# Performance work log

Hardware: AMD Instinct MI355X
Metric: run time of the kernel (lower is better)

## Reference

```python
import jax, jax.numpy as jnp
import numpy as np

N, T, E, H, V = 32768, 20, 50, 50, 200
PAD = 0

def setup_inputs() -> dict:
    key = jax.random.key(0)
    ks = jax.random.split(key, 11)
    s = 1.0 / np.sqrt(H)  # torch LSTM init scale
    return {
        "char_indices": jax.random.randint(ks[0], (N, T), 0, V, dtype=jnp.int32),
        "word_lengths": jax.random.randint(ks[1], (N,), 0, T + 1, dtype=jnp.int32),
        "emb": jax.random.normal(ks[2], (V, E), jnp.float32) * 0.1,
        "W_ih_f": jax.random.normal(ks[3], (4 * H, E), jnp.float32) * s,
        "W_hh_f": jax.random.normal(ks[4], (4 * H, H), jnp.float32) * s,
        "b_ih_f": jax.random.normal(ks[5], (4 * H,), jnp.float32) * s,
        "b_hh_f": jax.random.normal(ks[6], (4 * H,), jnp.float32) * s,
        "W_ih_b": jax.random.normal(ks[7], (4 * H, E), jnp.float32) * s,
        "W_hh_b": jax.random.normal(ks[8], (4 * H, H), jnp.float32) * s,
        "b_ih_b": jax.random.normal(ks[9], (4 * H,), jnp.float32) * s,
        "b_hh_b": jax.random.normal(ks[10], (4 * H,), jnp.float32) * s,
    }

def _run_dir(x, lengths, W_ih, W_hh, b_ih, b_hh, reverse):
    # x: [N,T,E]; returns final hidden state [N,H] at the word's true boundary.
    n = x.shape[0]
    xg = jnp.einsum('nte,ge->ntg', x, W_ih) + b_ih + b_hh  # [N,T,4H]
    def step(carry, t):
        h, c = carry
        g = xg[:, t] + h @ W_hh.T  # [N,4H]
        i, f, gg, o = jnp.split(g, 4, axis=-1)
        c_new = jax.nn.sigmoid(f) * c + jax.nn.sigmoid(i) * jnp.tanh(gg)
        h_new = jax.nn.sigmoid(o) * jnp.tanh(c_new)
        valid = (t < lengths)[:, None]  # only update inside the word
        return (jnp.where(valid, h_new, h), jnp.where(valid, c_new, c)), None
    ts = jnp.arange(T - 1, -1, -1) if reverse else jnp.arange(T)
    z = jnp.zeros((n, W_hh.shape[1]), x.dtype)
    (h, _), _ = jax.lax.scan(step, (z, z), ts)
    return h

def reference(char_indices, word_lengths, emb, W_ih_f, W_hh_f, b_ih_f, b_hh_f,
              W_ih_b, W_hh_b, b_ih_b, b_hh_b):
    emb = emb.at[PAD].set(0.0)  # padding_idx row is zero
    x = emb[char_indices]  # [N,T,E]
    h_f = _run_dir(x, word_lengths, W_ih_f, W_hh_f, b_ih_f, b_hh_f, reverse=False)
    h_b = _run_dir(x, word_lengths, W_ih_b, W_hh_b, b_ih_b, b_hh_b, reverse=True)
    return jnp.concatenate([h_f, h_b], axis=-1)  # [N, 2H]
```

## Files before the change

### kernel.cpp

```cpp
#include <hip/hip_runtime.h>


#define TT    20
#define HH    50
#define VV    200
#define TILES 13
#define GSTR  212
#define GSH   (VV * GSTR)
#define WSH   (TILES * 16 * 64)
#define NW    32768
#define NB_G  332
#define NB_W  104
#define NB_H  128

typedef __attribute__((ext_vector_type(8))) short bf16x8;
typedef __attribute__((ext_vector_type(4))) short s16x4;
typedef __attribute__((ext_vector_type(4))) float f32x4;

__device__ __forceinline__ float frcp(float x) { return __builtin_amdgcn_rcpf(x); }
__device__ __forceinline__ float fsig(float x) { return frcp(1.0f + __expf(-x)); }
__device__ __forceinline__ float ftanhf(float x) { return 1.0f - 2.0f * frcp(1.0f + __expf(2.0f * x)); }

__device__ __forceinline__ short f2bf(float x) {
    unsigned b = __builtin_bit_cast(unsigned, x);
    unsigned r = (b + 0x7FFFu + ((b >> 16) & 1u)) >> 16;
    return (short)r;
}
__device__ __forceinline__ float bf2f(short s) {
    return __builtin_bit_cast(float, ((unsigned)(unsigned short)s) << 16);
}

__global__ void k_prep(const float* __restrict__ emb,
                       const float* __restrict__ Wih_f, const float* __restrict__ bih_f,
                       const float* __restrict__ bhh_f,
                       const float* __restrict__ Wih_b, const float* __restrict__ bih_b,
                       const float* __restrict__ bhh_b,
                       const float* __restrict__ Whh_f, const float* __restrict__ Whh_b,
                       const int* __restrict__ lens,
                       short* __restrict__ Gimg, short* __restrict__ Wimg,
                       int* __restrict__ cnt) {
    int blk = blockIdx.x;
    int tid = threadIdx.x;
    if (blk < NB_G) {
        int idx = blk * 256 + tid;
        if (idx >= 2 * GSH) return;
        int d = idx / GSH;
        int rem = idx % GSH;
        int v = rem / GSTR;
        int u = (rem % GSTR) >> 2;
        int g = idx & 3;
        if (u >= HH) { Gimg[idx] = 0; return; }
        int r = g * HH + u;
        const float* Wih = d ? Wih_b : Wih_f;
        const float* bih = d ? bih_b : bih_f;
        const float* bhh = d ? bhh_b : bhh_f;
        float s = bih[r] + bhh[r];
        if (v != 0) {
            #pragma unroll 10
            for (int e = 0; e < HH; ++e) s = fmaf(emb[v * HH + e], Wih[r * HH + e], s);
        }
        Gimg[idx] = f2bf(s);
    } else if (blk < NB_G + NB_W) {
        int idx = (blk - NB_G) * 256 + tid;
        if (idx >= 2 * WSH) return;
        int d = idx / WSH;
        int e = idx % WSH;
        int t = e >> 10, m = (e >> 6) & 15, k = e & 63;
        int u = 4 * t + (m >> 2), g = m & 3;
        const float* Whh = d ? Whh_b : Whh_f;
        float val = (k < HH && u < HH) ? Whh[(g * HH + u) * HH + k] : 0.0f;
        int ksw = (k & 7) | (((k >> 3) ^ (m & 7)) << 3);
        Wimg[d * WSH + (e & ~63) + ksw] = f2bf(val);
    } else {
        int hb = blk - NB_G - NB_W;
        __shared__ int hcnt[21];
        if (tid < 21) hcnt[tid] = 0;
        __syncthreads();
        atomicAdd(&hcnt[lens[hb * 256 + tid]], 1);
        __syncthreads();
        if (tid < 21) cnt[hb * 21 + tid] = hcnt[tid];
    }
}

__global__ void k_scan(const int* __restrict__ cnt, int* __restrict__ offs) {
    __shared__ int tot[21], start[21];
    int t = threadIdx.x;
    if (t < 21) {
        int s = 0;
        for (int b = 0; b < NB_H; ++b) s += cnt[b * 21 + t];
        tot[t] = s;
    }
    __syncthreads();
    if (t == 0) {
        int acc = 0;
        for (int L = 20; L >= 0; --L) { start[L] = acc; acc += tot[L]; }
    }
    __syncthreads();
    if (t < 21) {
        int acc = start[t];
        for (int b = 0; b < NB_H; ++b) { offs[b * 21 + t] = acc; acc += cnt[b * 21 + t]; }
    }
}

__global__ void k_scat(const int* __restrict__ lens, const int* __restrict__ offs,
                       int* __restrict__ perm) {
    __shared__ int cur[21];
    int b = blockIdx.x, t = threadIdx.x;
    if (t < 21) cur[t] = offs[b * 21 + t];
    __syncthreads();
    int i = b * 256 + t;
    int pos = atomicAdd(&cur[lens[i]], 1);
    perm[pos] = i;
}

__launch_bounds__(512, 1)
__global__ void k_lstm(const int* __restrict__ chars, const int* __restrict__ lens,
                       const int* __restrict__ perm,
                       const short* __restrict__ Gimg, const short* __restrict__ Wimg,
                       float* __restrict__ out) {
    __shared__ __align__(16) short Wa[WSH];
    __shared__ __align__(16) short Gl[GSH];
    __shared__ __align__(16) short hs[8][1024];
    __shared__ unsigned char cs[8][320];

    int gb   = blockIdx.x;
    int d    = gb & 1;
    int grp  = gb >> 1;
    int tid  = threadIdx.x;
    int lane = tid & 63;
    int wv   = __builtin_amdgcn_readfirstlane(tid >> 6);
    int quad = lane >> 4;
    int n    = lane & 15;
    int x7   = n & 7;

    {
        const int4* src = (const int4*)(Wimg + d * WSH);
        int4* dst = (int4*)Wa;
        for (int i = tid; i < WSH / 8; i += 512) dst[i] = src[i];
    }
    {
        const int4* src = (const int4*)(Gimg + d * GSH);
        int4* dst = (int4*)Gl;
        for (int i = tid; i < GSH / 8; i += 512) dst[i] = src[i];
    }
    {
        int4 z = {0, 0, 0, 0};
        int4* hz = (int4*)&hs[0][0];
        for (int i = tid; i < 8 * 1024 / 8; i += 512) hz[i] = z;
    }
    int slotbase = (grp * 8 + wv) * 16;
    {
        for (int i = lane; i < 16 * TT; i += 64) {
            int w = perm[slotbase + i / TT];
            cs[wv][i] = (unsigned char)chars[w * TT + i % TT];
        }
    }
    __syncthreads();

    int word = perm[slotbase + n];
    int L = lens[word];
    int mL = L;
    #pragma unroll
    for (int off = 8; off; off >>= 1) {
        int t2 = __shfl_xor(mL, off);
        mL = mL > t2 ? mL : t2;
    }
    mL = __builtin_amdgcn_readfirstlane(mL);

    const bf16x8* ap = (const bf16x8*)Wa;
    const bf16x8* bp = (const bf16x8*)hs[wv];
    short* hw = hs[wv];
    const unsigned char* cw = cs[wv] + n * TT;

    int pa0 = quad ^ x7;
    int pa1 = (quad + 4) ^ x7;

    float cst[TILES], hf[TILES];
    #pragma unroll
    for (int t = 0; t < TILES; ++t) { cst[t] = 0.0f; hf[t] = 0.0f; }

    #pragma unroll 1
    for (int s = 0; s < mL; ++s) {
        bool valid = s < L;
        int p = valid ? (d ? (L - 1 - s) : s) : 0;
        int v = cw[p];

        bf16x8 B0 = bp[n * 8 + pa0];
        bf16x8 B1 = bp[n * 8 + pa1];

        f32x4 acc[TILES];
        #pragma unroll
        for (int t = 0; t < TILES; ++t) {
            int u = 4 * t + quad;
            s16x4 gv = *(const s16x4*)&Gl[v * GSTR + u * 4];
            f32x4 a;
            a[0] = bf2f(gv[0]); a[1] = bf2f(gv[1]);
            a[2] = bf2f(gv[2]); a[3] = bf2f(gv[3]);
            bf16x8 A0 = ap[(t * 16 + n) * 8 + pa0];
            bf16x8 A1 = ap[(t * 16 + n) * 8 + pa1];
            a = __builtin_amdgcn_mfma_f32_16x16x32_bf16(A0, B0, a, 0, 0, 0);
            a = __builtin_amdgcn_mfma_f32_16x16x32_bf16(A1, B1, a, 0, 0, 0);
            acc[t] = a;
        }
        #pragma unroll
        for (int t = 0; t < TILES; ++t) {
            int u = 4 * t + quad;
            float ig = fsig(acc[t][0]);
            float fg = fsig(acc[t][1]);
            float gg = ftanhf(acc[t][2]);
            float og = fsig(acc[t][3]);
            float cold = cst[t];
            float cn = fg * cold + ig * gg;
            float hn = og * ftanhf(cn);
            bool upd = valid && (u < HH);
            cst[t] = upd ? cn : cold;
            hf[t]  = upd ? hn : hf[t];
            if (upd) {
                int idx = n * 64 + (((u >> 3) ^ x7) << 3) + (u & 7);
                hw[idx] = f2bf(hn);
            }
        }
    }

    float* orow = out + (size_t)word * (2 * HH) + d * HH;
    #pragma unroll
    for (int t = 0; t < TILES; ++t) {
        int u = 4 * t + quad;
        if (u < HH) orow[u] = hf[t];
    }
}

extern "C" void kernel_launch(void* const* d_in, const int* in_sizes, int n_in,
                              void* d_out, int out_size, void* d_ws, size_t ws_size,
                              hipStream_t stream) {
    const int*   chars = (const int*)d_in[0];
    const int*   lens  = (const int*)d_in[1];
    const float* emb   = (const float*)d_in[2];
    const float* Wih_f = (const float*)d_in[3];
    const float* Whh_f = (const float*)d_in[4];
    const float* bih_f = (const float*)d_in[5];
    const float* bhh_f = (const float*)d_in[6];
    const float* Wih_b = (const float*)d_in[7];
    const float* Whh_b = (const float*)d_in[8];
    const float* bih_b = (const float*)d_in[9];
    const float* bhh_b = (const float*)d_in[10];
    float* out = (float*)d_out;

    short* Gimg = (short*)d_ws;
    short* Wimg = Gimg + 2 * GSH;
    int*   cnt  = (int*)(Wimg + 2 * WSH);
    int*   offs = cnt + NB_H * 21;
    int*   perm = offs + NB_H * 21;

    k_prep<<<NB_G + NB_W + NB_H, 256, 0, stream>>>(emb, Wih_f, bih_f, bhh_f,
                                                   Wih_b, bih_b, bhh_b,
                                                   Whh_f, Whh_b, lens,
                                                   Gimg, Wimg, cnt);
    k_scan<<<1, 64, 0, stream>>>(cnt, offs);
    k_scat<<<NB_H, 256, 0, stream>>>(lens, offs, perm);
    k_lstm<<<512, 512, 0, stream>>>(chars, lens, perm, Gimg, Wimg, out);
}
```

Before: 159.6 us.

## Fuse length-sort scan into scatter and double LSTM block size with interleaved groups

Removes the single-block k_scan launch. Each scatter block now computes its own prefix offsets directly from the per-block histogram counts. The LSTM kernel moves from 512 to 1024 threads per block, so each block handles 16 word groups and the grid covers every CU in a single round. Weight and gate tables are staged into LDS once per block instead of twice. Word groups are assigned to waves in an interleaved pattern across the length-sorted order, which mixes long and short words within a block for balance. The cost is more redundant count reads in the scatter blocks and a higher per-block LDS footprint.

```diff
diff --git a/kernel.cpp b/kernel.cpp
--- a/kernel.cpp
+++ b/kernel.cpp
@@ -82,50 +82,45 @@
     }
 }
 
-__global__ void k_scan(const int* __restrict__ cnt, int* __restrict__ offs) {
-    __shared__ int tot[21], start[21];
-    int t = threadIdx.x;
+__global__ void k_scat(const int* __restrict__ lens, const int* __restrict__ cnt,
+                       int* __restrict__ perm) {
+    __shared__ int tots[21], before_s[21], cur[21];
+    int b = blockIdx.x, t = threadIdx.x;
     if (t < 21) {
-        int s = 0;
-        for (int b = 0; b < NB_H; ++b) s += cnt[b * 21 + t];
-        tot[t] = s;
-    }
-    __syncthreads();
-    if (t == 0) {
-        int acc = 0;
-        for (int L = 20; L >= 0; --L) { start[L] = acc; acc += tot[L]; }
+        int before = 0, tot = 0;
+        for (int bb = 0; bb < NB_H; ++bb) {
+            int c = cnt[bb * 21 + t];
+            before += (bb < b) ? c : 0;
+            tot += c;
+        }
+        tots[t] = tot;
+        before_s[t] = before;
     }
     __syncthreads();
     if (t < 21) {
-        int acc = start[t];
-        for (int b = 0; b < NB_H; ++b) { offs[b * 21 + t] = acc; acc += cnt[b * 21 + t]; }
-    }
-}
-
-__global__ void k_scat(const int* __restrict__ lens, const int* __restrict__ offs,
-                       int* __restrict__ perm) {
-    __shared__ int cur[21];
-    int b = blockIdx.x, t = threadIdx.x;
-    if (t < 21) cur[t] = offs[b * 21 + t];
+        int start = 0;
+        for (int L = 20; L > t; --L) start += tots[L];
+        cur[t] = start + before_s[t];
+    }
     __syncthreads();
     int i = b * 256 + t;
     int pos = atomicAdd(&cur[lens[i]], 1);
     perm[pos] = i;
 }
 
-__launch_bounds__(512, 1)
+__launch_bounds__(1024, 4)
 __global__ void k_lstm(const int* __restrict__ chars, const int* __restrict__ lens,
                        const int* __restrict__ perm,
                        const short* __restrict__ Gimg, const short* __restrict__ Wimg,
                        float* __restrict__ out) {
     __shared__ __align__(16) short Wa[WSH];
     __shared__ __align__(16) short Gl[GSH];
-    __shared__ __align__(16) short hs[8][1024];
-    __shared__ unsigned char cs[8][320];
+    __shared__ __align__(16) short hs[16][1024];
+    __shared__ unsigned char cs[16][320];
 
     int gb   = blockIdx.x;
     int d    = gb & 1;
-    int grp  = gb >> 1;
+    int b    = gb >> 1;
     int tid  = threadIdx.x;
     int lane = tid & 63;
     int wv   = __builtin_amdgcn_readfirstlane(tid >> 6);
@@ -136,19 +131,20 @@
     {
         const int4* src = (const int4*)(Wimg + d * WSH);
         int4* dst = (int4*)Wa;
-        for (int i = tid; i < WSH / 8; i += 512) dst[i] = src[i];
+        for (int i = tid; i < WSH / 8; i += 1024) dst[i] = src[i];
     }
     {
         const int4* src = (const int4*)(Gimg + d * GSH);
         int4* dst = (int4*)Gl;
-        for (int i = tid; i < GSH / 8; i += 512) dst[i] = src[i];
+        for (int i = tid; i < GSH / 8; i += 1024) dst[i] = src[i];
     }
     {
         int4 z = {0, 0, 0, 0};
         int4* hz = (int4*)&hs[0][0];
-        for (int i = tid; i < 8 * 1024 / 8; i += 512) hz[i] = z;
-    }
-    int slotbase = (grp * 8 + wv) * 16;
+        for (int i = tid; i < 16 * 1024 / 8; i += 1024) hz[i] = z;
+    }
+    int g = wv * 128 + b;
+    int slotbase = g * 16;
     {
         for (int i = lane; i < 16 * TT; i += 64) {
             int w = perm[slotbase + i / TT];
@@ -249,14 +245,12 @@
     short* Gimg = (short*)d_ws;
     short* Wimg = Gimg + 2 * GSH;
     int*   cnt  = (int*)(Wimg + 2 * WSH);
-    int*   offs = cnt + NB_H * 21;
-    int*   perm = offs + NB_H * 21;
+    int*   perm = cnt + NB_H * 21;
 
     k_prep<<<NB_G + NB_W + NB_H, 256, 0, stream>>>(emb, Wih_f, bih_f, bhh_f,
                                                    Wih_b, bih_b, bhh_b,
                                                    Whh_f, Whh_b, lens,
                                                    Gimg, Wimg, cnt);
-    k_scan<<<1, 64, 0, stream>>>(cnt, offs);
-    k_scat<<<NB_H, 256, 0, stream>>>(lens, offs, perm);
-    k_lstm<<<512, 512, 0, stream>>>(chars, lens, perm, Gimg, Wimg, out);
-}
+    k_scat<<<NB_H, 256, 0, stream>>>(lens, cnt, perm);
+    k_lstm<<<256, 1024, 0, stream>>>(chars, lens, perm, Gimg, Wimg, out);
+}
```

Result: slower. 323.1 us (+102.4%).
